# Kernel optimization log

Measured on AMD Instinct MI355X. Metric: run time of the kernel, lower is better.

The kernel has to match this reference:

```python
import jax, jax.numpy as jnp
import numpy as np
from jax import lax

B, C, N, T, K = 16, 64, 512, 64, 3
EPS = 1e-5


def _bn(x, g, b):
    # training-mode BatchNorm2d over (B, H=N, W=T) per channel
    m = jnp.mean(x, axis=(0, 2, 3), keepdims=True)
    v = jnp.var(x, axis=(0, 2, 3), keepdims=True)
    return (x - m) * lax.rsqrt(v + EPS) * g[None, :, None, None] + b[None, :, None, None]


def _conv(x, w, b, pad):
    y = lax.conv_general_dilated(x, w, (1, 1), ((0, 0), pad),
                                 dimension_numbers=('NCHW', 'OIHW', 'NCHW'))
    return y + b[None, :, None, None]


def setup_inputs() -> dict:
    key = jax.random.key(0)
    ks = jax.random.split(key, 8)
    xav = lambda k, sh, fi, fo: jax.random.normal(k, sh, jnp.float32) * np.sqrt(2.0 / (fi + fo))
    return {
        'x': jax.random.normal(ks[0], (B, C, N, T), jnp.float32),
        'adj_mx': jax.random.normal(ks[1], (K, N, N), jnp.float32) / np.sqrt(N),
        'cheb_w': xav(ks[2], (K, C, C), C, C),
        'cheb_b': jnp.zeros((C,), jnp.float32),
        'w1': xav(ks[3], (C, C, 1, 3), 3 * C, 3 * C),
        'b1': jnp.zeros((C,), jnp.float32),
        'g1': jnp.ones((C,), jnp.float32),
        'be1': jnp.zeros((C,), jnp.float32),
        'w2': xav(ks[4], (C, C, 1, 3), 3 * C, 3 * C),
        'b2': jnp.zeros((C,), jnp.float32),
        'g2': jnp.ones((C,), jnp.float32),
        'be2': jnp.zeros((C,), jnp.float32),
        'gate_w': xav(ks[5], (C, 2 * C, 1, 1), 2 * C, C),
        'gate_b': jnp.zeros((C,), jnp.float32),
        'res_w': xav(ks[6], (C, C, 1, 1), C, C),
        'res_b': jnp.zeros((C,), jnp.float32),
        'g3': jnp.ones((C,), jnp.float32),
        'be3': jnp.zeros((C,), jnp.float32),
    }


def _forward(x, adj_mx, cheb_w, cheb_b, w1, b1, g1, be1, w2, b2, g2, be2,
             gate_w, gate_b, res_w, res_b, g3, be3):
    # ChebFilterBlock: out[b,o,n,t] = sum_{k,i,m} x[b,i,m,t] adj[k,m,n] W[k,i,o] + bias
    spatial = jnp.einsum('bimt,kmn,kio->bont', x, adj_mx, cheb_w) \
              + cheb_b[None, :, None, None]
    # temporal branch: two (1,3) convs with BN+ReLU
    t = jax.nn.relu(_bn(_conv(x, w1, b1, (1, 1)), g1, be1))
    t = jax.nn.relu(_bn(_conv(t, w2, b2, (1, 1)), g2, be2))
    # gated fusion
    comb = jnp.concatenate([spatial, t], axis=1)
    gate = jax.nn.sigmoid(_conv(comb, gate_w, gate_b, (0, 0)))
    res = _conv(x, res_w, res_b, (0, 0))
    out = gate * spatial + (1.0 - gate) * t + res
    return _bn(out, g3, be3)


def reference(x, adj_mx, cheb_w, cheb_b, w1, b1, g1, be1, w2, b2, g2, be2,
              gate_w, gate_b, res_w, res_b, g3, be3):
    return _forward(x, adj_mx, cheb_w, cheb_b, w1, b1, g1, be1, w2, b2, g2, be2,
                    gate_w, gate_b, res_w, res_b, g3, be3)
```

## Files before the change

kernel.cpp:

```cpp
#include <hip/hip_runtime.h>
#include <hip/hip_bf16.h>
#include <cstdint>

#define BB 16
#define CC 64
#define NN 512
#define TT 64
#define KCH 3
#define PP (BB*NN*TT)
#define EPSB 1e-5f

typedef __bf16 bf16;
typedef __bf16 bf16x8 __attribute__((ext_vector_type(8)));
typedef __bf16 bf16x4 __attribute__((ext_vector_type(4)));
typedef float  f32x4  __attribute__((ext_vector_type(4)));

#define MFMA16(A,Bv,Cv) __builtin_amdgcn_mfma_f32_16x16x32_bf16((A),(Bv),(Cv),0,0,0)

__device__ __forceinline__ void gload_lds16(const bf16* g, bf16* l){
  __builtin_amdgcn_global_load_lds(
      (const __attribute__((address_space(1))) void*)g,
      (__attribute__((address_space(3))) void*)l, 16, 0, 0);
}

__global__ __launch_bounds__(256) void k_prep(const float* __restrict__ adj,
    const float* __restrict__ w1, const float* __restrict__ w2,
    const float* __restrict__ cw, const float* __restrict__ gw,
    const float* __restrict__ rw, bf16* __restrict__ adjb,
    bf16* __restrict__ w1p, bf16* __restrict__ w2p, bf16* __restrict__ cp,
    bf16* __restrict__ gp, bf16* __restrict__ rp){
  int blk = blockIdx.x, tid = threadIdx.x;
  if (blk < 3072){
    int idx = blk*256 + tid;
    int m = idx & 511, n = (idx >> 9) & 511, k = idx >> 18;
    adjb[idx] = (bf16)adj[((size_t)(k*512 + m))*512 + n];
    return;
  }
  int e0 = (blk - 3072)*256 + tid;
  if (e0 < 12288){
    int e = e0;
    int j = e&7, lane = (e>>3)&63, cf = (e>>9)&3, ks = e>>11;
    int k = ks*32 + (lane>>4)*8 + j, col = cf*16 + (lane&15);
    int kk = k >> 6, i = k & 63;
    w1p[e] = (bf16)w1[(col*64 + i)*3 + kk];
    w2p[e] = (bf16)w2[(col*64 + i)*3 + kk];
    cp[e]  = (bf16)cw[((size_t)kk*64 + i)*64 + col];
  } else if (e0 < 20480){
    int e = e0 - 12288;
    int j = e&7, lane = (e>>3)&63, cf = (e>>9)&3, ks = e>>11;
    int k = ks*32 + (lane>>4)*8 + j, col = cf*16 + (lane&15);
    gp[e] = (bf16)gw[col*128 + k];
  } else {
    int e = e0 - 20480;
    int j = e&7, lane = (e>>3)&63, cf = (e>>9)&3, ks = e>>11;
    int k = ks*32 + (lane>>4)*8 + j, col = cf*16 + (lane&15);
    rp[e] = (bf16)rw[col*64 + k];
  }
}

__global__ __launch_bounds__(256) void k_xprep(const float* __restrict__ x,
    bf16* __restrict__ xlb, bf16* __restrict__ xmt){
  __shared__ bf16 T[32768];
  int bid = blockIdx.x;
  int b = bid >> 6, i0 = ((bid >> 3) & 7)*8, n0 = (bid & 7)*64;
  int tid = threadIdx.x;
  #pragma unroll 4
  for (int it = 0; it < 32; ++it){
    int flat = it*256 + tid;
    int t4 = flat & 15, n = (flat >> 4) & 63, i = flat >> 10;
    float4 v = *reinterpret_cast<const float4*>(
        x + ((size_t)((b*64 + i0 + i)*512) + (n0 + n))*64 + t4*4);
    int s = t4 ^ ((n + 2*i) & 15);
    bf16x4 pk; pk[0]=(bf16)v.x; pk[1]=(bf16)v.y; pk[2]=(bf16)v.z; pk[3]=(bf16)v.w;
    *reinterpret_cast<bf16x4*>(&T[(i*64 + n)*64 + s*4]) = pk;
  }
  __syncthreads();
  #pragma unroll 4
  for (int it = 0; it < 16; ++it){
    int flat = it*256 + tid;
    int mc = flat & 7, i = (flat >> 3) & 7, t = flat >> 6;
    bf16x8 o;
    #pragma unroll
    for (int e = 0; e < 8; ++e){
      int m = mc*8 + e;
      int s = (t >> 2) ^ ((m + 2*i) & 15);
      o[e] = T[(i*64 + m)*64 + s*4 + (t & 3)];
    }
    *reinterpret_cast<bf16x8*>(
        &xmt[((size_t)((b*64 + t)*64) + i0 + i)*512 + n0 + mc*8]) = o;
  }
  #pragma unroll 4
  for (int it = 0; it < 16; ++it){
    int flat = it*256 + tid;
    int t = flat & 63, n = flat >> 6;
    bf16x8 o;
    #pragma unroll
    for (int e = 0; e < 8; ++e){
      int s = (t >> 2) ^ ((n + 2*e) & 15);
      o[e] = T[(e*64 + n)*64 + s*4 + (t & 3)];
    }
    *reinterpret_cast<bf16x8*>(
        &xlb[(((size_t)b*512 + n0 + n)*64 + t)*64 + i0]) = o;
  }
}

__global__ __launch_bounds__(256,4) void k_conv(const bf16* __restrict__ in,
    const bf16* __restrict__ wp, bf16* __restrict__ outp, float* __restrict__ part,
    const float* __restrict__ sc, const float* __restrict__ sh){
  int tid = threadIdx.x, w = tid >> 6, l = tid & 63, l15 = l & 15, lg = l >> 4;
  int blk = blockIdx.x;
  size_t rowbase = (size_t)blk * 64;
  const bf16* xr = in + rowbase * 64;
  int t = w*16 + l15;
  f32x4 acc[4] = {};
  #pragma unroll
  for (int ks = 0; ks < 6; ++ks){
    int dt = ks >> 1, kh = ks & 1;
    int ts = t + dt - 1;
    bf16x8 a = {};
    if (ts >= 0 && ts < 64){
      a = *reinterpret_cast<const bf16x8*>(xr + ts*64 + kh*32 + lg*8);
      if (sc){
        int i0 = kh*32 + lg*8;
        #pragma unroll
        for (int e = 0; e < 8; ++e){
          float f = (float)a[e]*sc[i0+e] + sh[i0+e];
          a[e] = (bf16)fmaxf(f, 0.f);
        }
      }
    }
    #pragma unroll
    for (int cf = 0; cf < 4; ++cf){
      bf16x8 bfr = *reinterpret_cast<const bf16x8*>(wp + ((ks*4 + cf)*64 + l)*8);
      acc[cf] = MFMA16(a, bfr, acc[cf]);
    }
  }
  __shared__ float ssum[4][4][16], ssq[4][4][16];
  #pragma unroll
  for (int cf = 0; cf < 4; ++cf){
    int o = cf*16 + l15;
    float s = 0.f, q = 0.f;
    #pragma unroll
    for (int r = 0; r < 4; ++r){
      float vv = acc[cf][r];
      int to = w*16 + lg*4 + r;
      outp[(rowbase + to)*64 + o] = (bf16)vv;
      s += vv; q += vv*vv;
    }
    s += __shfl_xor(s, 16); s += __shfl_xor(s, 32);
    q += __shfl_xor(q, 16); q += __shfl_xor(q, 32);
    if (lg == 0){ ssum[w][cf][l15] = s; ssq[w][cf][l15] = q; }
  }
  __syncthreads();
  if (tid < 64){
    int cf = tid >> 4, c = tid & 15;
    float s = ssum[0][cf][c]+ssum[1][cf][c]+ssum[2][cf][c]+ssum[3][cf][c];
    float q = ssq[0][cf][c]+ssq[1][cf][c]+ssq[2][cf][c]+ssq[3][cf][c];
    part[(size_t)blk*128 + tid*2]     = s;
    part[(size_t)blk*128 + tid*2 + 1] = q;
  }
}

__global__ __launch_bounds__(256) void k_stats(const float* __restrict__ part, int nb,
    const float* __restrict__ g, const float* __restrict__ be,
    float* __restrict__ sc, float* __restrict__ sh){
  int c = blockIdx.x, tid = threadIdx.x;
  float s = 0.f, q = 0.f;
  for (int i = tid; i < nb; i += 256){
    s += part[(size_t)i*128 + c*2];
    q += part[(size_t)i*128 + c*2 + 1];
  }
  __shared__ float rs[256], rq[256];
  rs[tid] = s; rq[tid] = q; __syncthreads();
  for (int st = 128; st > 0; st >>= 1){
    if (tid < st){ rs[tid] += rs[tid+st]; rq[tid] += rq[tid+st]; }
    __syncthreads();
  }
  if (tid == 0){
    float cnt = (float)PP;
    float mean = rs[0]/cnt, var = rq[0]/cnt - mean*mean;
    float r = rsqrtf(var + EPSB);
    sc[c] = g[c]*r;
    sh[c] = be[c] - mean*g[c]*r;
  }
}

__global__ __launch_bounds__(512,4) void k_gemm1(const bf16* __restrict__ xmt,
    const bf16* __restrict__ adjb, const bf16* __restrict__ cp,
    const float* __restrict__ cb, bf16* __restrict__ spm){
  __shared__ bf16 As[3][4096];
  __shared__ bf16 Bs[3][4096];
  __shared__ bf16 VT[128*128];

  int tid = threadIdx.x, w = tid >> 6, l = tid & 63, l15 = l & 15, lg = l >> 4;
  int wr = w >> 2, wc = w & 3;

  int orig = blockIdx.x;
  int wg = (orig & 7) * 256 + (orig >> 3);
  int jt = wg >> 2, nt = wg & 3;
  int J0 = jt*128, N0 = nt*128;

  const bf16* aglob = xmt + (size_t)J0*512;
  const bf16* bbase = adjb + (size_t)N0*512;

  int sr = tid >> 2, sc = tid & 3;
  int scg = sc ^ (sr & 3) ^ ((sr >> 2) & 3);
  size_t soff = (size_t)sr*512 + scg*8;

  auto stage = [&](int t){
    int buf = t % 3;
    const bf16* bg = bbase + (size_t)(t >> 4)*(512*512);
    int m0 = (t & 15)*32;
    gload_lds16(aglob + soff + m0, &As[buf][tid*8]);
    gload_lds16(bg    + soff + m0, &Bs[buf][tid*8]);
  };

  int aoff[4], boff[2];
  #pragma unroll
  for (int rf = 0; rf < 4; ++rf){
    int row = wr*64 + rf*16 + l15;
    aoff[rf] = row*32 + ((lg ^ (row & 3) ^ ((row >> 2) & 3))*8);
  }
  #pragma unroll
  for (int cf = 0; cf < 2; ++cf){
    int row = wc*32 + cf*16 + l15;
    boff[cf] = row*32 + ((lg ^ (row & 3) ^ ((row >> 2) & 3))*8);
  }

  f32x4 acc[4][2] = {};
  f32x4 acc2[2][4] = {};

  stage(0); stage(1);
  for (int t = 0; t < 48; ++t){
    asm volatile("s_waitcnt lgkmcnt(0)" ::: "memory");
    __builtin_amdgcn_sched_barrier(0);
    __builtin_amdgcn_s_barrier();
    if (t < 46) stage(t+2);
    if (t < 46)       asm volatile("s_waitcnt vmcnt(4)" ::: "memory");
    else if (t == 46) asm volatile("s_waitcnt vmcnt(2)" ::: "memory");
    else              asm volatile("s_waitcnt vmcnt(0)" ::: "memory");
    __builtin_amdgcn_sched_barrier(0);

    int buf = t % 3;
    bf16x8 a[4], bb[2];
    #pragma unroll
    for (int rf = 0; rf < 4; ++rf)
      a[rf] = *reinterpret_cast<const bf16x8*>(&As[buf][aoff[rf]]);
    #pragma unroll
    for (int cf = 0; cf < 2; ++cf)
      bb[cf] = *reinterpret_cast<const bf16x8*>(&Bs[buf][boff[cf]]);
    #pragma unroll
    for (int rf = 0; rf < 4; ++rf)
      #pragma unroll
      for (int cf = 0; cf < 2; ++cf)
        acc[rf][cf] = MFMA16(a[rf], bb[cf], acc[rf][cf]);

    if ((t & 15) == 15){
      int kk = t >> 4;
      #pragma unroll
      for (int rf = 0; rf < 4; ++rf){
        int jb = wr*8 + rf*2 + (lg >> 1);
        #pragma unroll
        for (int cf = 0; cf < 2; ++cf){
          int nh = wc*32 + cf*16 + l15;
          bf16x4 pk;
          #pragma unroll
          for (int r = 0; r < 4; ++r) pk[r] = (bf16)acc[rf][cf][r];
          *reinterpret_cast<bf16x4*>(
              &VT[nh*128 + ((jb ^ (nh & 15)) << 3) + ((lg & 1) << 2)]) = pk;
          acc[rf][cf] = (f32x4){0.f, 0.f, 0.f, 0.f};
        }
      }
      asm volatile("s_waitcnt lgkmcnt(0)" ::: "memory");
      __builtin_amdgcn_sched_barrier(0);
      __builtin_amdgcn_s_barrier();

      #pragma unroll
      for (int ks2 = 0; ks2 < 2; ++ks2){
        bf16x8 bc[4];
        #pragma unroll
        for (int cf = 0; cf < 4; ++cf)
          bc[cf] = *reinterpret_cast<const bf16x8*>(
              cp + (((kk*2 + ks2)*4 + cf)*64 + l)*8);
        #pragma unroll
        for (int h = 0; h < 2; ++h){
          int nh = h*64 + (w & 3)*16 + l15;
          int jb = (w >> 2)*8 + ks2*4 + lg;
          bf16x8 a2 = *reinterpret_cast<const bf16x8*>(
              &VT[nh*128 + ((jb ^ (nh & 15)) << 3)]);
          #pragma unroll
          for (int cf = 0; cf < 4; ++cf)
            acc2[h][cf] = MFMA16(a2, bc[cf], acc2[h][cf]);
        }
      }
    }
  }

  __syncthreads();
  bf16* SP = VT;
  float cbv[4];
  #pragma unroll
  for (int cf = 0; cf < 4; ++cf) cbv[cf] = cb[cf*16 + l15];
  int b = jt >> 5, t0 = (jt & 31)*2;
  #pragma unroll
  for (int h = 0; h < 2; ++h){
    int rowb = (w >> 2)*128 + h*64 + (w & 3)*16 + lg*4;
    #pragma unroll
    for (int cf = 0; cf < 4; ++cf){
      int o = cf*16 + l15;
      #pragma unroll
      for (int r = 0; r < 4; ++r)
        SP[(rowb + r)*64 + o] = (bf16)(acc2[h][cf][r] + cbv[cf]);
    }
  }
  __syncthreads();
  #pragma unroll
  for (int q = 0; q < 4; ++q){
    int flat = q*512 + tid;
    int row = flat >> 3, oc = (flat & 7)*8;
    int tl = row >> 7, n = row & 127;
    bf16x8 vv = *reinterpret_cast<const bf16x8*>(&SP[row*64 + oc]);
    *reinterpret_cast<bf16x8*>(
        &spm[(((size_t)b*512 + N0 + n)*64 + (t0 + tl))*64 + oc]) = vv;
  }
}

__global__ __launch_bounds__(256,4) void k_fusion(const bf16* __restrict__ spm,
    const bf16* __restrict__ t2, const bf16* __restrict__ xlb,
    const bf16* __restrict__ gp, const bf16* __restrict__ rp,
    const float* __restrict__ sc2, const float* __restrict__ sh2,
    const float* __restrict__ gateb, bf16* __restrict__ pre,
    float* __restrict__ part){
  int tid = threadIdx.x, w = tid >> 6, l = tid & 63, l15 = l & 15, lg = l >> 4;
  int blk = blockIdx.x;
  int b = blk >> 9, n = blk & 511;
  size_t rowbase = (size_t)blk * 64;
  int t = w*16 + l15;
  f32x4 ag[4] = {}, ar[4] = {};
  #pragma unroll
  for (int ks = 0; ks < 4; ++ks){
    bf16x8 a;
    if (ks < 2){
      a = *reinterpret_cast<const bf16x8*>(spm + (rowbase + t)*64 + ks*32 + lg*8);
    } else {
      int i0 = (ks-2)*32 + lg*8;
      bf16x8 raw = *reinterpret_cast<const bf16x8*>(t2 + (rowbase + t)*64 + i0);
      #pragma unroll
      for (int e = 0; e < 8; ++e){
        float f = (float)raw[e]*sc2[i0+e] + sh2[i0+e];
        a[e] = (bf16)fmaxf(f, 0.f);
      }
    }
    #pragma unroll
    for (int cf = 0; cf < 4; ++cf){
      bf16x8 bfr = *reinterpret_cast<const bf16x8*>(gp + ((ks*4 + cf)*64 + l)*8);
      ag[cf] = MFMA16(a, bfr, ag[cf]);
    }
  }
  #pragma unroll
  for (int ks = 0; ks < 2; ++ks){
    bf16x8 a = *reinterpret_cast<const bf16x8*>(xlb + (rowbase + t)*64 + ks*32 + lg*8);
    #pragma unroll
    for (int cf = 0; cf < 4; ++cf){
      bf16x8 bfr = *reinterpret_cast<const bf16x8*>(rp + ((ks*4 + cf)*64 + l)*8);
      ar[cf] = MFMA16(a, bfr, ar[cf]);
    }
  }
  __shared__ float ssum[4][4][16], ssq[4][4][16];
  int tb = w*16 + lg*4;
  #pragma unroll
  for (int cf = 0; cf < 4; ++cf){
    int o = cf*16 + l15;
    float gb = gateb[o], sco = sc2[o], sho = sh2[o];
    float s = 0.f, q = 0.f;
    bf16x4 ov;
    #pragma unroll
    for (int r = 0; r < 4; ++r){
      size_t row = rowbase + tb + r;
      float z = ag[cf][r] + gb;
      float g = 1.f/(1.f + __expf(-z));
      float spv = (float)spm[row*64 + o];
      float tv  = (float)t2[row*64 + o];
      tv = fmaxf(tv*sco + sho, 0.f);
      float val = g*spv + (1.f - g)*tv + ar[cf][r];
      ov[r] = (bf16)val;
      s += val; q += val*val;
    }
    *reinterpret_cast<bf16x4*>(pre + (((size_t)b*64 + o)*512 + n)*64 + tb) = ov;
    s += __shfl_xor(s, 16); s += __shfl_xor(s, 32);
    q += __shfl_xor(q, 16); q += __shfl_xor(q, 32);
    if (lg == 0){ ssum[w][cf][l15] = s; ssq[w][cf][l15] = q; }
  }
  __syncthreads();
  if (tid < 64){
    int cf = tid >> 4, c = tid & 15;
    float s = ssum[0][cf][c]+ssum[1][cf][c]+ssum[2][cf][c]+ssum[3][cf][c];
    float q = ssq[0][cf][c]+ssq[1][cf][c]+ssq[2][cf][c]+ssq[3][cf][c];
    part[(size_t)blk*128 + tid*2]     = s;
    part[(size_t)blk*128 + tid*2 + 1] = q;
  }
}

__global__ __launch_bounds__(256) void k_bn3(const bf16* __restrict__ pre,
    float* __restrict__ out,
    const float* __restrict__ sc, const float* __restrict__ sh){
  size_t total8 = (size_t)BB*CC*NN*TT/8;
  for (size_t i8 = (size_t)blockIdx.x*256 + threadIdx.x; i8 < total8;
       i8 += (size_t)gridDim.x*256){
    bf16x8 v = reinterpret_cast<const bf16x8*>(pre)[i8];
    int o = (int)(i8 >> 12) & 63;
    float a = sc[o], bsh = sh[o];
    float4 r0, r1;
    r0.x = (float)v[0]*a + bsh; r0.y = (float)v[1]*a + bsh;
    r0.z = (float)v[2]*a + bsh; r0.w = (float)v[3]*a + bsh;
    r1.x = (float)v[4]*a + bsh; r1.y = (float)v[5]*a + bsh;
    r1.z = (float)v[6]*a + bsh; r1.w = (float)v[7]*a + bsh;
    reinterpret_cast<float4*>(out)[i8*2]     = r0;
    reinterpret_cast<float4*>(out)[i8*2 + 1] = r1;
  }
}

extern "C" void kernel_launch(void* const* d_in, const int* in_sizes, int n_in,
                              void* d_out, int out_size, void* d_ws, size_t ws_size,
                              hipStream_t stream){
  (void)in_sizes; (void)n_in; (void)out_size; (void)ws_size;
  const float* x   = (const float*)d_in[0];
  const float* adj = (const float*)d_in[1];
  const float* cw  = (const float*)d_in[2];
  const float* cb  = (const float*)d_in[3];
  const float* w1  = (const float*)d_in[4];
  const float* g1  = (const float*)d_in[6];
  const float* be1 = (const float*)d_in[7];
  const float* w2  = (const float*)d_in[8];
  const float* g2  = (const float*)d_in[10];
  const float* be2 = (const float*)d_in[11];
  const float* gw  = (const float*)d_in[12];
  const float* gb  = (const float*)d_in[13];
  const float* rw  = (const float*)d_in[14];
  const float* g3  = (const float*)d_in[16];
  const float* be3 = (const float*)d_in[17];
  float* out = (float*)d_out;

  char* ws = (char*)d_ws;
  size_t off = 0;
  auto alloc = [&](size_t bytes)->char*{
    char* p = ws + off; off += (bytes + 255) & ~(size_t)255; return p;
  };
  bf16* xlb  = (bf16*)alloc((size_t)PP*64*2);
  bf16* xmt  = (bf16*)alloc((size_t)PP*64*2);
  bf16* t1   = (bf16*)alloc((size_t)PP*64*2);
  bf16* t2   = (bf16*)alloc((size_t)PP*64*2);
  bf16* spm  = t1;
  bf16* pre  = xmt;
  bf16* adjb = (bf16*)alloc((size_t)KCH*512*512*2);
  bf16* w1p  = (bf16*)alloc(6*2048*2);
  bf16* w2p  = (bf16*)alloc(6*2048*2);
  bf16* cp   = (bf16*)alloc(6*2048*2);
  bf16* gp   = (bf16*)alloc(4*2048*2);
  bf16* rp   = (bf16*)alloc(2*2048*2);
  float* part = (float*)alloc((size_t)8192*128*4);
  float* s1sc = (float*)alloc(256); float* s1sh = (float*)alloc(256);
  float* s2sc = (float*)alloc(256); float* s2sh = (float*)alloc(256);
  float* s3sc = (float*)alloc(256); float* s3sh = (float*)alloc(256);

  k_prep <<<dim3(3168), dim3(256), 0, stream>>>(adj, w1, w2, cw, gw, rw,
                                                adjb, w1p, w2p, cp, gp, rp);
  k_xprep<<<dim3(1024), dim3(256), 0, stream>>>(x, xlb, xmt);

  k_conv <<<dim3(8192), dim3(256), 0, stream>>>(xlb, w1p, t1, part, nullptr, nullptr);
  k_stats<<<dim3(64),   dim3(256), 0, stream>>>(part, 8192, g1, be1, s1sc, s1sh);
  k_conv <<<dim3(8192), dim3(256), 0, stream>>>(t1, w2p, t2, part, s1sc, s1sh);
  k_stats<<<dim3(64),   dim3(256), 0, stream>>>(part, 8192, g2, be2, s2sc, s2sh);

  k_gemm1<<<dim3(2048), dim3(512), 0, stream>>>(xmt, adjb, cp, cb, spm);

  k_fusion<<<dim3(8192), dim3(256), 0, stream>>>(spm, t2, xlb, gp, rp,
                                                 s2sc, s2sh, gb, pre, part);
  k_stats<<<dim3(64),   dim3(256), 0, stream>>>(part, 8192, g3, be3, s3sc, s3sh);
  k_bn3  <<<dim3(2048), dim3(256), 0, stream>>>(pre, out, s3sc, s3sh);
}
```

Baseline: 544.4 us.

## Load GEMM1 operands directly from global into registers using 32x32 MFMA

Removes the LDS triple-buffered async staging of the x and adjacency tiles in the first GEMM. Each wave now loads its operand fragments straight from global memory into registers, double-buffered in software, and uses 32x32x16 MFMA instead of 16x16x32. Launch bounds drop to 2 blocks per CU to make room for the extra registers. Fragments are no longer shared across waves through LDS, so global and L2 traffic goes up and occupancy goes down.

```diff
diff --git a/kernel.cpp b/kernel.cpp
--- a/kernel.cpp
+++ b/kernel.cpp
@@ -14,14 +14,10 @@
 typedef __bf16 bf16x8 __attribute__((ext_vector_type(8)));
 typedef __bf16 bf16x4 __attribute__((ext_vector_type(4)));
 typedef float  f32x4  __attribute__((ext_vector_type(4)));
+typedef float  f32x16 __attribute__((ext_vector_type(16)));
 
 #define MFMA16(A,Bv,Cv) __builtin_amdgcn_mfma_f32_16x16x32_bf16((A),(Bv),(Cv),0,0,0)
-
-__device__ __forceinline__ void gload_lds16(const bf16* g, bf16* l){
-  __builtin_amdgcn_global_load_lds(
-      (const __attribute__((address_space(1))) void*)g,
-      (__attribute__((address_space(3))) void*)l, 16, 0, 0);
-}
+#define MFMA32(A,Bv,Cv) __builtin_amdgcn_mfma_f32_32x32x16_bf16((A),(Bv),(Cv),0,0,0)
 
 __global__ __launch_bounds__(256) void k_prep(const float* __restrict__ adj,
     const float* __restrict__ w1, const float* __restrict__ w2,
@@ -185,113 +181,94 @@
   }
 }
 
-__global__ __launch_bounds__(512,4) void k_gemm1(const bf16* __restrict__ xmt,
+__global__ __launch_bounds__(512,2) void k_gemm1(const bf16* __restrict__ xmt,
     const bf16* __restrict__ adjb, const bf16* __restrict__ cp,
     const float* __restrict__ cb, bf16* __restrict__ spm){
-  __shared__ bf16 As[3][4096];
-  __shared__ bf16 Bs[3][4096];
   __shared__ bf16 VT[128*128];
 
   int tid = threadIdx.x, w = tid >> 6, l = tid & 63, l15 = l & 15, lg = l >> 4;
-  int wr = w >> 2, wc = w & 3;
+  int l31 = l & 31, lh = l >> 5;
+  int wjt = w >> 1, wn = w & 1;
 
   int orig = blockIdx.x;
   int wg = (orig & 7) * 256 + (orig >> 3);
   int jt = wg >> 2, nt = wg & 3;
   int J0 = jt*128, N0 = nt*128;
 
-  const bf16* aglob = xmt + (size_t)J0*512;
-  const bf16* bbase = adjb + (size_t)N0*512;
-
-  int sr = tid >> 2, sc = tid & 3;
-  int scg = sc ^ (sr & 3) ^ ((sr >> 2) & 3);
-  size_t soff = (size_t)sr*512 + scg*8;
-
-  auto stage = [&](int t){
-    int buf = t % 3;
-    const bf16* bg = bbase + (size_t)(t >> 4)*(512*512);
-    int m0 = (t & 15)*32;
-    gload_lds16(aglob + soff + m0, &As[buf][tid*8]);
-    gload_lds16(bg    + soff + m0, &Bs[buf][tid*8]);
-  };
-
-  int aoff[4], boff[2];
-  #pragma unroll
-  for (int rf = 0; rf < 4; ++rf){
-    int row = wr*64 + rf*16 + l15;
-    aoff[rf] = row*32 + ((lg ^ (row & 3) ^ ((row >> 2) & 3))*8);
-  }
-  #pragma unroll
-  for (int cf = 0; cf < 2; ++cf){
-    int row = wc*32 + cf*16 + l15;
-    boff[cf] = row*32 + ((lg ^ (row & 3) ^ ((row >> 2) & 3))*8);
-  }
-
-  f32x4 acc[4][2] = {};
+  const bf16* arow = xmt + (size_t)(J0 + wjt*32 + l31)*512 + lh*8;
+  const bf16* brow0 = adjb + (size_t)(N0 + wn*64 + l31)*512 + lh*8;
+  const bf16* brow1 = brow0 + (size_t)32*512;
+
+  f32x16 acc0, acc1;
   f32x4 acc2[2][4] = {};
 
-  stage(0); stage(1);
-  for (int t = 0; t < 48; ++t){
-    asm volatile("s_waitcnt lgkmcnt(0)" ::: "memory");
-    __builtin_amdgcn_sched_barrier(0);
-    __builtin_amdgcn_s_barrier();
-    if (t < 46) stage(t+2);
-    if (t < 46)       asm volatile("s_waitcnt vmcnt(4)" ::: "memory");
-    else if (t == 46) asm volatile("s_waitcnt vmcnt(2)" ::: "memory");
-    else              asm volatile("s_waitcnt vmcnt(0)" ::: "memory");
-    __builtin_amdgcn_sched_barrier(0);
-
-    int buf = t % 3;
-    bf16x8 a[4], bb[2];
-    #pragma unroll
-    for (int rf = 0; rf < 4; ++rf)
-      a[rf] = *reinterpret_cast<const bf16x8*>(&As[buf][aoff[rf]]);
-    #pragma unroll
-    for (int cf = 0; cf < 2; ++cf)
-      bb[cf] = *reinterpret_cast<const bf16x8*>(&Bs[buf][boff[cf]]);
-    #pragma unroll
-    for (int rf = 0; rf < 4; ++rf)
-      #pragma unroll
-      for (int cf = 0; cf < 2; ++cf)
-        acc[rf][cf] = MFMA16(a[rf], bb[cf], acc[rf][cf]);
-
-    if ((t & 15) == 15){
-      int kk = t >> 4;
-      #pragma unroll
-      for (int rf = 0; rf < 4; ++rf){
-        int jb = wr*8 + rf*2 + (lg >> 1);
+  for (int kk = 0; kk < 3; ++kk){
+    size_t ko = (size_t)kk*512*512;
+    #pragma unroll
+    for (int e = 0; e < 16; ++e){ acc0[e] = 0.f; acc1[e] = 0.f; }
+
+    bf16x8 aC[4], b0C[4], b1C[4], aN[4], b0N[4], b1N[4];
+    #pragma unroll
+    for (int s = 0; s < 4; ++s){
+      aC[s]  = *reinterpret_cast<const bf16x8*>(arow  + s*16);
+      b0C[s] = *reinterpret_cast<const bf16x8*>(brow0 + ko + s*16);
+      b1C[s] = *reinterpret_cast<const bf16x8*>(brow1 + ko + s*16);
+    }
+    #pragma unroll
+    for (int t = 0; t < 8; ++t){
+      if (t < 7){
+        int m0 = (t+1)*64;
         #pragma unroll
-        for (int cf = 0; cf < 2; ++cf){
-          int nh = wc*32 + cf*16 + l15;
-          bf16x4 pk;
-          #pragma unroll
-          for (int r = 0; r < 4; ++r) pk[r] = (bf16)acc[rf][cf][r];
-          *reinterpret_cast<bf16x4*>(
-              &VT[nh*128 + ((jb ^ (nh & 15)) << 3) + ((lg & 1) << 2)]) = pk;
-          acc[rf][cf] = (f32x4){0.f, 0.f, 0.f, 0.f};
+        for (int s = 0; s < 4; ++s){
+          aN[s]  = *reinterpret_cast<const bf16x8*>(arow  + m0 + s*16);
+          b0N[s] = *reinterpret_cast<const bf16x8*>(brow0 + ko + m0 + s*16);
+          b1N[s] = *reinterpret_cast<const bf16x8*>(brow1 + ko + m0 + s*16);
         }
       }
-      asm volatile("s_waitcnt lgkmcnt(0)" ::: "memory");
-      __builtin_amdgcn_sched_barrier(0);
-      __builtin_amdgcn_s_barrier();
-
-      #pragma unroll
-      for (int ks2 = 0; ks2 < 2; ++ks2){
-        bf16x8 bc[4];
+      #pragma unroll
+      for (int s = 0; s < 4; ++s){
+        acc0 = MFMA32(aC[s], b0C[s], acc0);
+        acc1 = MFMA32(aC[s], b1C[s], acc1);
+      }
+      if (t < 7){
+        #pragma unroll
+        for (int s = 0; s < 4; ++s){ aC[s] = aN[s]; b0C[s] = b0N[s]; b1C[s] = b1N[s]; }
+      }
+    }
+
+    __syncthreads();
+    #pragma unroll
+    for (int nt32 = 0; nt32 < 2; ++nt32){
+      int nh = wn*64 + nt32*32 + l31;
+      f32x16 av = nt32 ? acc1 : acc0;
+      #pragma unroll
+      for (int g = 0; g < 4; ++g){
+        int jb = wjt*4 + g;
+        bf16x4 pk;
+        #pragma unroll
+        for (int r = 0; r < 4; ++r) pk[r] = (bf16)av[g*4 + r];
+        *reinterpret_cast<bf16x4*>(
+            &VT[nh*128 + ((jb ^ (nh & 15)) << 3) + (lh << 2)]) = pk;
+      }
+    }
+    __syncthreads();
+
+    #pragma unroll
+    for (int ks2 = 0; ks2 < 2; ++ks2){
+      bf16x8 bc[4];
+      #pragma unroll
+      for (int cf = 0; cf < 4; ++cf)
+        bc[cf] = *reinterpret_cast<const bf16x8*>(
+            cp + (((kk*2 + ks2)*4 + cf)*64 + l)*8);
+      #pragma unroll
+      for (int h = 0; h < 2; ++h){
+        int nh = h*64 + (w & 3)*16 + l15;
+        int jb = (w >> 2)*8 + ks2*4 + lg;
+        bf16x8 a2 = *reinterpret_cast<const bf16x8*>(
+            &VT[nh*128 + ((jb ^ (nh & 15)) << 3)]);
         #pragma unroll
         for (int cf = 0; cf < 4; ++cf)
-          bc[cf] = *reinterpret_cast<const bf16x8*>(
-              cp + (((kk*2 + ks2)*4 + cf)*64 + l)*8);
-        #pragma unroll
-        for (int h = 0; h < 2; ++h){
-          int nh = h*64 + (w & 3)*16 + l15;
-          int jb = (w >> 2)*8 + ks2*4 + lg;
-          bf16x8 a2 = *reinterpret_cast<const bf16x8*>(
-              &VT[nh*128 + ((jb ^ (nh & 15)) << 3)]);
-          #pragma unroll
-          for (int cf = 0; cf < 4; ++cf)
-            acc2[h][cf] = MFMA16(a2, bc[cf], acc2[h][cf]);
-        }
+          acc2[h][cf] = MFMA16(a2, bc[cf], acc2[h][cf]);
       }
     }
   }
```

Result: slower. 805.2 us (+47.9%).
